# Optimization experiments

Hardware: AMD Instinct MI355X
Metric: run time of the kernel (lower is better)

Reference implementation:

```python
import jax, jax.numpy as jnp
import numpy as np

EPS = 0.001
FLOW_WARP_WEIGHT = 1.0
_GRAY_W = jnp.array([0.299, 0.587, 0.114], dtype=jnp.float32)


def _to_gray(img):
    # img: [B, 3, H, W] -> [B, 1, H, W] luminance
    return jnp.einsum('bchw,c->bhw', img, _GRAY_W.astype(img.dtype))[:, None]


def _resize_bilinear_align_corners(x, h_out, w_out):
    # x: [B, C, H, W] -> [B, C, h_out, w_out], bilinear, align_corners=True
    B, C, H, W = x.shape
    sy = jnp.arange(h_out, dtype=x.dtype) * ((H - 1) / max(h_out - 1, 1))
    sx = jnp.arange(w_out, dtype=x.dtype) * ((W - 1) / max(w_out - 1, 1))
    y0 = jnp.floor(sy).astype(jnp.int32)
    x0 = jnp.floor(sx).astype(jnp.int32)
    y1 = jnp.minimum(y0 + 1, H - 1)
    x1 = jnp.minimum(x0 + 1, W - 1)
    wy = (sy - y0)[:, None]            # [h_out, 1]
    wx = (sx - x0)[None, :]            # [1, w_out]
    # interp along H
    xh = x[:, :, y0, :] * (1.0 - wy)[..., None].squeeze(-1)[None, None] if False else x[:, :, y0, :] * (1.0 - wy) + x[:, :, y1, :] * wy  # [B,C,h_out,W]
    # interp along W
    out = xh[:, :, :, x0] * (1.0 - wx) + xh[:, :, :, x1] * wx
    return out


def _resize_flow_to_image(flow, h_img, w_img):
    flow_uv = flow[:, :2]
    fh, fw = flow_uv.shape[-2:]
    if (fh, fw) == (h_img, w_img):
        return flow_uv
    r = _resize_bilinear_align_corners(flow_uv, h_img, w_img)
    scale = jnp.array([w_img / max(fw, 1), h_img / max(fh, 1)], dtype=flow.dtype)
    return r * scale[None, :, None, None]


def _bilinear_sample_zeros(img, gx, gy):
    # img: [B, 1, H, W]; gx, gy: [B, H, W] pixel coords (align_corners=True)
    B, _, H, W = img.shape
    x0f = jnp.floor(gx)
    y0f = jnp.floor(gy)
    wx = gx - x0f
    wy = gy - y0f
    x0 = x0f.astype(jnp.int32)
    y0 = y0f.astype(jnp.int32)
    b = jnp.arange(B)[:, None, None]

    def gather(yi, xi):
        valid = (xi >= 0) & (xi <= W - 1) & (yi >= 0) & (yi <= H - 1)
        v = img[b, 0, jnp.clip(yi, 0, H - 1), jnp.clip(xi, 0, W - 1)]
        return jnp.where(valid, v, jnp.zeros((), img.dtype))

    v00 = gather(y0, x0)
    v01 = gather(y0, x0 + 1)
    v10 = gather(y0 + 1, x0)
    v11 = gather(y0 + 1, x0 + 1)
    out = (v00 * (1 - wx) * (1 - wy) + v01 * wx * (1 - wy)
           + v10 * (1 - wx) * wy + v11 * wx * wy)
    return out[:, None]  # [B,1,H,W]


def _forward(pred_prev, pred_next, flow_prev_to_next):
    prev_g = _to_gray(pred_prev)   # [B,1,H,W]
    next_g = _to_gray(pred_next)
    B, _, H, W = prev_g.shape
    flow_uv = _resize_flow_to_image(flow_prev_to_next, H, W)  # [B,2,H,W]
    yy, xx = jnp.meshgrid(jnp.arange(H, dtype=prev_g.dtype),
                          jnp.arange(W, dtype=prev_g.dtype), indexing='ij')
    gx = xx[None] + flow_uv[:, 0]  # [B,H,W]
    gy = yy[None] + flow_uv[:, 1]
    valid = ((gx >= 0) & (gx <= W - 1) & (gy >= 0) & (gy <= H - 1)).astype(prev_g.dtype)
    warped = _bilinear_sample_zeros(next_g, gx, gy)  # [B,1,H,W]
    diff = prev_g - warped
    valid_mask = valid[:, None]
    valid_count = jnp.maximum(valid_mask.sum(), 1.0)
    loss_map = jnp.sqrt(diff * diff + EPS * EPS) * valid_mask
    loss = loss_map.sum() / valid_count
    return FLOW_WARP_WEIGHT * loss, loss


def setup_inputs() -> dict:
    key = jax.random.key(0)
    k1, k2, k3 = jax.random.split(key, 3)
    pred_prev = jax.random.uniform(k1, (16, 3, 512, 512), dtype=jnp.float32)
    pred_next = jax.random.uniform(k2, (16, 3, 512, 512), dtype=jnp.float32)
    flow = jax.random.normal(k3, (16, 2, 128, 128), dtype=jnp.float32)
    return {"pred_prev": pred_prev, "pred_next": pred_next, "flow_prev_to_next": flow}


def reference(pred_prev, pred_next, flow_prev_to_next):
    return _forward(pred_prev, pred_next, flow_prev_to_next)
```

## Files before the change

kernel.cpp:

```cpp
#include <hip/hip_runtime.h>


typedef _Float16 half4v __attribute__((ext_vector_type(4)));

constexpr int B  = 16;
constexpr int H  = 512;
constexpr int W  = 512;
constexpr int FH = 128;
constexpr int FW = 128;
constexpr int HW  = H * W;
constexpr int IMG = 3 * HW;
constexpr int FHW = FH * FW;
constexpr float EPS = 0.001f;

constexpr int TX = 64, TY = 32;
constexpr int TW = 120, TH = 80;
constexpr int FROWS  = 10;
constexpr int FLOW_F = 2 * FROWS * FW;

constexpr int NB = 2048;

__device__ __forceinline__ float gray3(const float* __restrict__ img, int off) {
    return 0.299f * img[off] + 0.587f * img[HW + off] + 0.114f * img[2 * HW + off];
}

__global__ __launch_bounds__(256) void loss_kernel(
    const float* __restrict__ prev, const float* __restrict__ nxt,
    const float* __restrict__ flow, double* __restrict__ psum,
    unsigned int* __restrict__ pcnt)
{
    __shared__ __align__(16) _Float16 smh[TW * TH];
    __shared__ __align__(16) float    smf[FLOW_F];

    const int bid = ((blockIdx.x & 7) << 8) | (blockIdx.x >> 3);
    const int b   = bid >> 7;
    const int t   = bid & 127;
    const int tx  = t & 7;
    const int ty  = t >> 3;
    const int x0t = tx * TX;
    const int y0t = ty * TY;

    const float fr = (float)(127.0 / 511.0);
    const int fy_lo = (int)((float)y0t * fr);

    const float* __restrict__ nb = nxt + (long)b * IMG;

    for (int it = threadIdx.x; it < TH * (TW / 4); it += 256) {
        const int r  = it / (TW / 4), c = it - r * (TW / 4);
        const int sy = y0t - 24 + r;
        const int sx = x0t - 24 + c * 4;
        half4v hv = (half4v)0;
        if ((unsigned)sy < (unsigned)H && (unsigned)sx <= (unsigned)(W - 4)) {
            const float* __restrict__ p = nb + sy * W + sx;
            const float4 rr = *(const float4*)(p);
            const float4 gg = *(const float4*)(p + HW);
            const float4 bl = *(const float4*)(p + 2 * HW);
            hv[0] = (_Float16)(0.299f * rr.x + 0.587f * gg.x + 0.114f * bl.x);
            hv[1] = (_Float16)(0.299f * rr.y + 0.587f * gg.y + 0.114f * bl.y);
            hv[2] = (_Float16)(0.299f * rr.z + 0.587f * gg.z + 0.114f * bl.z);
            hv[3] = (_Float16)(0.299f * rr.w + 0.587f * gg.w + 0.114f * bl.w);
        }
        *(half4v*)(smh + r * TW + c * 4) = hv;
    }
    {
        const float* __restrict__ fsrc = flow + (long)b * 2 * FHW;
        for (int it = threadIdx.x; it < 2 * FROWS * (FW / 4); it += 256) {
            const int c    = it / (FROWS * (FW / 4));
            const int rr   = (it - c * (FROWS * (FW / 4))) >> 5;
            const int c4   = it & 31;
            const int frow = min(fy_lo + rr, FH - 1);
            const float4 v = *(const float4*)(fsrc + c * FHW + frow * FW + c4 * 4);
            *(float4*)(smf + c * (FROWS * FW) + rr * FW + c4 * 4) = v;
        }
    }

    const int xq = threadIdx.x & 15;
    const int yl = threadIdx.x >> 4;
    const int xb = x0t + xq * 4;

    float pg[2][4];
    #pragma unroll
    for (int k = 0; k < 2; ++k) {
        const int y = y0t + yl + k * 16;
        const float* __restrict__ pb = prev + (long)b * IMG + y * W + xb;
        const float4 pr  = *(const float4*)(pb);
        const float4 pgc = *(const float4*)(pb + HW);
        const float4 plc = *(const float4*)(pb + 2 * HW);
        pg[k][0] = 0.299f * pr.x + 0.587f * pgc.x + 0.114f * plc.x;
        pg[k][1] = 0.299f * pr.y + 0.587f * pgc.y + 0.114f * plc.y;
        pg[k][2] = 0.299f * pr.z + 0.587f * pgc.z + 0.114f * plc.z;
        pg[k][3] = 0.299f * pr.w + 0.587f * pgc.w + 0.114f * plc.w;
    }

    __syncthreads();

    const float sxfb = (float)xb * fr;
    const int F  = (int)sxfb;
    const int F2 = min(F + 2, FW - 1);

    double lsum = 0.0;
    unsigned int lcnt = 0;

    #pragma unroll
    for (int k = 0; k < 2; ++k) {
        const int y = y0t + yl + k * 16;

        const float syf = (float)y * fr;
        const int   fy0 = (int)syf;
        const float wy  = syf - (float)fy0;
        const int r0 = fy0 - fy_lo;
        const int r1 = min(fy0 + 1, FH - 1) - fy_lo;

        const float* __restrict__ su = smf;
        const float* __restrict__ sv = smf + FROWS * FW;
        const float u0a = su[r0 * FW + F], u0b = su[r0 * FW + F + 1], u0c = su[r0 * FW + F2];
        const float u1a = su[r1 * FW + F], u1b = su[r1 * FW + F + 1], u1c = su[r1 * FW + F2];
        const float v0a = sv[r0 * FW + F], v0b = sv[r0 * FW + F + 1], v0c = sv[r0 * FW + F2];
        const float v1a = sv[r1 * FW + F], v1b = sv[r1 * FW + F + 1], v1c = sv[r1 * FW + F2];

        #pragma unroll
        for (int i = 0; i < 4; ++i) {
            const int x = xb + i;
            const float sxf = (float)x * fr;
            const int   fx0 = (int)sxf;
            const float wx  = sxf - (float)fx0;
            const int   d   = fx0 - F;

            const float u00 = d ? u0b : u0a, u01 = d ? u0c : u0b;
            const float u10 = d ? u1b : u1a, u11 = d ? u1c : u1b;
            const float v00 = d ? v0b : v0a, v01 = d ? v0c : v0b;
            const float v10 = d ? v1b : v1a, v11 = d ? v1c : v1b;

            const float uc0 = u00 * (1.0f - wy) + u10 * wy;
            const float uc1 = u01 * (1.0f - wy) + u11 * wy;
            const float vc0 = v00 * (1.0f - wy) + v10 * wy;
            const float vc1 = v01 * (1.0f - wy) + v11 * wy;
            const float u = (uc0 * (1.0f - wx) + uc1 * wx) * 4.0f;
            const float v = (vc0 * (1.0f - wx) + vc1 * wx) * 4.0f;

            const float gx = (float)x + u;
            const float gy = (float)y + v;
            const float vm = ((gx >= 0.0f) & (gx <= (float)(W - 1)) &
                              (gy >= 0.0f) & (gy <= (float)(H - 1))) ? 1.0f : 0.0f;

            const float gxf = floorf(gx), gyf = floorf(gy);
            const float wwx = gx - gxf,  wwy = gy - gyf;
            const int ix0 = (int)gxf, iy0 = (int)gyf;

            const int cx = ix0 - (x0t - 24);
            const int ry = iy0 - (y0t - 24);
            float c00, c01, c10, c11;
            if ((unsigned)cx <= (unsigned)(TW - 2) && (unsigned)ry <= (unsigned)(TH - 2)) {
                const int la = ry * TW + cx;
                c00 = (float)smh[la];      c01 = (float)smh[la + 1];
                c10 = (float)smh[la + TW]; c11 = (float)smh[la + TW + 1];
            } else {
                const bool vx0g = (ix0 >= 0) & (ix0 < W);
                const bool vx1g = (ix0 + 1 >= 0) & (ix0 + 1 < W);
                const bool vy0g = (iy0 >= 0) & (iy0 < H);
                const bool vy1g = (iy0 + 1 >= 0) & (iy0 + 1 < H);
                const int xc0 = min(max(ix0, 0), W - 1), xc1 = min(max(ix0 + 1, 0), W - 1);
                const int yc0 = min(max(iy0, 0), H - 1), yc1 = min(max(iy0 + 1, 0), H - 1);
                c00 = (vy0g & vx0g) ? gray3(nb, yc0 * W + xc0) : 0.0f;
                c01 = (vy0g & vx1g) ? gray3(nb, yc0 * W + xc1) : 0.0f;
                c10 = (vy1g & vx0g) ? gray3(nb, yc1 * W + xc0) : 0.0f;
                c11 = (vy1g & vx1g) ? gray3(nb, yc1 * W + xc1) : 0.0f;
            }

            const float warped = c00 * (1.0f - wwx) * (1.0f - wwy)
                               + c01 * wwx * (1.0f - wwy)
                               + c10 * (1.0f - wwx) * wwy
                               + c11 * wwx * wwy;
            const float diff = pg[k][i] - warped;
            const float l = sqrtf(diff * diff + EPS * EPS);
            lsum += (double)(l * vm);
            lcnt += (unsigned int)vm;
        }
    }

    #pragma unroll
    for (int off = 32; off > 0; off >>= 1) {
        lsum += __shfl_down(lsum, off);
        lcnt += __shfl_down(lcnt, off);
    }
    __shared__ double s_sum[4];
    __shared__ unsigned int s_cnt[4];
    const int wid = threadIdx.x >> 6, lane = threadIdx.x & 63;
    if (lane == 0) { s_sum[wid] = lsum; s_cnt[wid] = lcnt; }
    __syncthreads();
    if (threadIdx.x == 0) {
        psum[blockIdx.x] = s_sum[0] + s_sum[1] + s_sum[2] + s_sum[3];
        pcnt[blockIdx.x] = s_cnt[0] + s_cnt[1] + s_cnt[2] + s_cnt[3];
    }
}

__global__ __launch_bounds__(256) void reduce_kernel(
    const double* __restrict__ psum, const unsigned int* __restrict__ pcnt,
    int nb, float* __restrict__ out)
{
    double s = 0.0;
    unsigned long long c = 0;
    for (int i = threadIdx.x; i < nb; i += 256) {
        s += psum[i];
        c += (unsigned long long)pcnt[i];
    }
    #pragma unroll
    for (int off = 32; off > 0; off >>= 1) {
        s += __shfl_down(s, off);
        c += __shfl_down(c, off);
    }
    __shared__ double ss[4];
    __shared__ unsigned long long sc[4];
    const int wid = threadIdx.x >> 6, lane = threadIdx.x & 63;
    if (lane == 0) { ss[wid] = s; sc[wid] = c; }
    __syncthreads();
    if (threadIdx.x == 0) {
        double ts = ss[0] + ss[1] + ss[2] + ss[3];
        double tc = (double)(sc[0] + sc[1] + sc[2] + sc[3]);
        if (tc < 1.0) tc = 1.0;
        const float loss = (float)(ts / tc);
        out[0] = loss;
        out[1] = loss;
    }
}

extern "C" void kernel_launch(void* const* d_in, const int* in_sizes, int n_in,
                              void* d_out, int out_size, void* d_ws, size_t ws_size,
                              hipStream_t stream) {
    const float* prev = (const float*)d_in[0];
    const float* nxt  = (const float*)d_in[1];
    const float* flow = (const float*)d_in[2];
    float* out = (float*)d_out;

    double* psum = (double*)d_ws;
    unsigned int* pcnt = (unsigned int*)((char*)d_ws + NB * 8);

    loss_kernel<<<dim3(NB), dim3(256), 0, stream>>>(prev, nxt, flow, psum, pcnt);
    reduce_kernel<<<dim3(1), dim3(256), 0, stream>>>(psum, pcnt, NB, out);
}
```

Baseline: 44.02 us.

## Precompute padded fp16 grayscale of next frame in separate kernel

```diff
diff --git a/kernel.cpp b/kernel.cpp
--- a/kernel.cpp
+++ b/kernel.cpp
@@ -1,7 +1,7 @@
 #include <hip/hip_runtime.h>
 
 
-typedef _Float16 half4v __attribute__((ext_vector_type(4)));
+typedef _Float16 half8 __attribute__((ext_vector_type(8)));
 
 constexpr int B  = 16;
 constexpr int H  = 512;
@@ -13,24 +13,53 @@
 constexpr int FHW = FH * FW;
 constexpr float EPS = 0.001f;
 
+constexpr int P    = 32;
+constexpr int PW   = W + 2 * P;
+constexpr int PH   = H + 2 * P;
+constexpr int PIMG = PW * PH;
+constexpr int PQ8  = PH * (PW / 8);
+
 constexpr int TX = 64, TY = 32;
-constexpr int TW = 120, TH = 80;
-constexpr int FROWS  = 10;
-constexpr int FLOW_F = 2 * FROWS * FW;
+constexpr int TW = 104, TH = 64;
+constexpr int FROWS = 10;
+constexpr int FCOLS = 24;
 
 constexpr int NB = 2048;
 
-__device__ __forceinline__ float gray3(const float* __restrict__ img, int off) {
-    return 0.299f * img[off] + 0.587f * img[HW + off] + 0.114f * img[2 * HW + off];
+__global__ __launch_bounds__(256) void pad_gray_kernel(
+    const float* __restrict__ nxt, _Float16* __restrict__ g)
+{
+    const int q  = blockIdx.x * 256 + threadIdx.x;
+    const int b  = q / PQ8;
+    const int r  = q - b * PQ8;
+    const int py = r / (PW / 8);
+    const int qx = r - py * (PW / 8);
+    const int y  = py - P;
+    const int xs = qx * 8 - P;
+    half8 o = (half8)0;
+    if ((unsigned)y < (unsigned)H && (unsigned)xs <= (unsigned)(W - 8)) {
+        const float* __restrict__ nb = nxt + (long)b * IMG + y * W + xs;
+        #pragma unroll
+        for (int h = 0; h < 2; ++h) {
+            const float4 rr = *(const float4*)(nb + 4 * h);
+            const float4 gg = *(const float4*)(nb + HW + 4 * h);
+            const float4 bl = *(const float4*)(nb + 2 * HW + 4 * h);
+            o[4 * h + 0] = (_Float16)(0.299f * rr.x + 0.587f * gg.x + 0.114f * bl.x);
+            o[4 * h + 1] = (_Float16)(0.299f * rr.y + 0.587f * gg.y + 0.114f * bl.y);
+            o[4 * h + 2] = (_Float16)(0.299f * rr.z + 0.587f * gg.z + 0.114f * bl.z);
+            o[4 * h + 3] = (_Float16)(0.299f * rr.w + 0.587f * gg.w + 0.114f * bl.w);
+        }
+    }
+    *(half8*)(g + (long)b * PIMG + py * PW + qx * 8) = o;
 }
 
 __global__ __launch_bounds__(256) void loss_kernel(
-    const float* __restrict__ prev, const float* __restrict__ nxt,
+    const float* __restrict__ prev, const _Float16* __restrict__ gpad,
     const float* __restrict__ flow, double* __restrict__ psum,
     unsigned int* __restrict__ pcnt)
 {
     __shared__ __align__(16) _Float16 smh[TW * TH];
-    __shared__ __align__(16) float    smf[FLOW_F];
+    __shared__ __align__(16) float    smf[2 * FROWS * FCOLS];
 
     const int bid = ((blockIdx.x & 7) << 8) | (blockIdx.x >> 3);
     const int b   = bid >> 7;
@@ -42,35 +71,25 @@
 
     const float fr = (float)(127.0 / 511.0);
     const int fy_lo = (int)((float)y0t * fr);
-
-    const float* __restrict__ nb = nxt + (long)b * IMG;
-
-    for (int it = threadIdx.x; it < TH * (TW / 4); it += 256) {
-        const int r  = it / (TW / 4), c = it - r * (TW / 4);
-        const int sy = y0t - 24 + r;
-        const int sx = x0t - 24 + c * 4;
-        half4v hv = (half4v)0;
-        if ((unsigned)sy < (unsigned)H && (unsigned)sx <= (unsigned)(W - 4)) {
-            const float* __restrict__ p = nb + sy * W + sx;
-            const float4 rr = *(const float4*)(p);
-            const float4 gg = *(const float4*)(p + HW);
-            const float4 bl = *(const float4*)(p + 2 * HW);
-            hv[0] = (_Float16)(0.299f * rr.x + 0.587f * gg.x + 0.114f * bl.x);
-            hv[1] = (_Float16)(0.299f * rr.y + 0.587f * gg.y + 0.114f * bl.y);
-            hv[2] = (_Float16)(0.299f * rr.z + 0.587f * gg.z + 0.114f * bl.z);
-            hv[3] = (_Float16)(0.299f * rr.w + 0.587f * gg.w + 0.114f * bl.w);
-        }
-        *(half4v*)(smh + r * TW + c * 4) = hv;
-    }
+    const int c0    = min((int)((float)x0t * fr) & ~3, FW - FCOLS);
+
+    const _Float16* __restrict__ gb = gpad + (long)b * PIMG;
+
     {
+        const _Float16* __restrict__ src = gb + (y0t - 16 + P) * PW + (x0t - 16 + P);
+        for (int it = threadIdx.x; it < TH * (TW / 8); it += 256) {
+            const int r = it / (TW / 8), c = it - r * (TW / 8);
+            *(uint4*)(smh + r * TW + c * 8) = *(const uint4*)(src + r * PW + c * 8);
+        }
         const float* __restrict__ fsrc = flow + (long)b * 2 * FHW;
-        for (int it = threadIdx.x; it < 2 * FROWS * (FW / 4); it += 256) {
-            const int c    = it / (FROWS * (FW / 4));
-            const int rr   = (it - c * (FROWS * (FW / 4))) >> 5;
-            const int c4   = it & 31;
+        for (int it = threadIdx.x; it < 2 * FROWS * (FCOLS / 4); it += 256) {
+            const int comp = it / (FROWS * (FCOLS / 4));
+            const int rem  = it - comp * (FROWS * (FCOLS / 4));
+            const int rr   = rem / (FCOLS / 4);
+            const int c4   = rem - rr * (FCOLS / 4);
             const int frow = min(fy_lo + rr, FH - 1);
-            const float4 v = *(const float4*)(fsrc + c * FHW + frow * FW + c4 * 4);
-            *(float4*)(smf + c * (FROWS * FW) + rr * FW + c4 * 4) = v;
+            const float4 v = *(const float4*)(fsrc + comp * FHW + frow * FW + c0 + c4 * 4);
+            *(float4*)(smf + comp * (FROWS * FCOLS) + rr * FCOLS + c4 * 4) = v;
         }
     }
 
@@ -95,8 +114,9 @@
     __syncthreads();
 
     const float sxfb = (float)xb * fr;
-    const int F  = (int)sxfb;
-    const int F2 = min(F + 2, FW - 1);
+    const int F   = (int)sxfb;
+    const int Fl  = F - c0;
+    const int F2l = min(F + 2, FW - 1) - c0;
 
     double lsum = 0.0;
     unsigned int lcnt = 0;
@@ -112,11 +132,11 @@
         const int r1 = min(fy0 + 1, FH - 1) - fy_lo;
 
         const float* __restrict__ su = smf;
-        const float* __restrict__ sv = smf + FROWS * FW;
-        const float u0a = su[r0 * FW + F], u0b = su[r0 * FW + F + 1], u0c = su[r0 * FW + F2];
-        const float u1a = su[r1 * FW + F], u1b = su[r1 * FW + F + 1], u1c = su[r1 * FW + F2];
-        const float v0a = sv[r0 * FW + F], v0b = sv[r0 * FW + F + 1], v0c = sv[r0 * FW + F2];
-        const float v1a = sv[r1 * FW + F], v1b = sv[r1 * FW + F + 1], v1c = sv[r1 * FW + F2];
+        const float* __restrict__ sv = smf + FROWS * FCOLS;
+        const float u0a = su[r0 * FCOLS + Fl], u0b = su[r0 * FCOLS + Fl + 1], u0c = su[r0 * FCOLS + F2l];
+        const float u1a = su[r1 * FCOLS + Fl], u1b = su[r1 * FCOLS + Fl + 1], u1c = su[r1 * FCOLS + F2l];
+        const float v0a = sv[r0 * FCOLS + Fl], v0b = sv[r0 * FCOLS + Fl + 1], v0c = sv[r0 * FCOLS + F2l];
+        const float v1a = sv[r1 * FCOLS + Fl], v1b = sv[r1 * FCOLS + Fl + 1], v1c = sv[r1 * FCOLS + F2l];
 
         #pragma unroll
         for (int i = 0; i < 4; ++i) {
@@ -147,24 +167,19 @@
             const float wwx = gx - gxf,  wwy = gy - gyf;
             const int ix0 = (int)gxf, iy0 = (int)gyf;
 
-            const int cx = ix0 - (x0t - 24);
-            const int ry = iy0 - (y0t - 24);
+            const int cx = ix0 - (x0t - 16);
+            const int ry = iy0 - (y0t - 16);
             float c00, c01, c10, c11;
             if ((unsigned)cx <= (unsigned)(TW - 2) && (unsigned)ry <= (unsigned)(TH - 2)) {
                 const int la = ry * TW + cx;
                 c00 = (float)smh[la];      c01 = (float)smh[la + 1];
                 c10 = (float)smh[la + TW]; c11 = (float)smh[la + TW + 1];
             } else {
-                const bool vx0g = (ix0 >= 0) & (ix0 < W);
-                const bool vx1g = (ix0 + 1 >= 0) & (ix0 + 1 < W);
-                const bool vy0g = (iy0 >= 0) & (iy0 < H);
-                const bool vy1g = (iy0 + 1 >= 0) & (iy0 + 1 < H);
-                const int xc0 = min(max(ix0, 0), W - 1), xc1 = min(max(ix0 + 1, 0), W - 1);
-                const int yc0 = min(max(iy0, 0), H - 1), yc1 = min(max(iy0 + 1, 0), H - 1);
-                c00 = (vy0g & vx0g) ? gray3(nb, yc0 * W + xc0) : 0.0f;
-                c01 = (vy0g & vx1g) ? gray3(nb, yc0 * W + xc1) : 0.0f;
-                c10 = (vy1g & vx0g) ? gray3(nb, yc1 * W + xc0) : 0.0f;
-                c11 = (vy1g & vx1g) ? gray3(nb, yc1 * W + xc1) : 0.0f;
+                const int iyc = min(max(iy0, -P), PH - P - 2);
+                const int ixc = min(max(ix0, -P), PW - P - 2);
+                const _Float16* __restrict__ gp = gb + (iyc + P) * PW + (ixc + P);
+                c00 = (float)gp[0];  c01 = (float)gp[1];
+                c10 = (float)gp[PW]; c11 = (float)gp[PW + 1];
             }
 
             const float warped = c00 * (1.0f - wwx) * (1.0f - wwy)
@@ -196,11 +211,11 @@
 
 __global__ __launch_bounds__(256) void reduce_kernel(
     const double* __restrict__ psum, const unsigned int* __restrict__ pcnt,
-    int nb, float* __restrict__ out)
+    float* __restrict__ out)
 {
     double s = 0.0;
     unsigned long long c = 0;
-    for (int i = threadIdx.x; i < nb; i += 256) {
+    for (int i = threadIdx.x; i < NB; i += 256) {
         s += psum[i];
         c += (unsigned long long)pcnt[i];
     }
@@ -215,7 +230,7 @@
     if (lane == 0) { ss[wid] = s; sc[wid] = c; }
     __syncthreads();
     if (threadIdx.x == 0) {
-        double ts = ss[0] + ss[1] + ss[2] + ss[3];
+        const double ts = ss[0] + ss[1] + ss[2] + ss[3];
         double tc = (double)(sc[0] + sc[1] + sc[2] + sc[3]);
         if (tc < 1.0) tc = 1.0;
         const float loss = (float)(ts / tc);
@@ -234,7 +249,9 @@
 
     double* psum = (double*)d_ws;
     unsigned int* pcnt = (unsigned int*)((char*)d_ws + NB * 8);
-
-    loss_kernel<<<dim3(NB), dim3(256), 0, stream>>>(prev, nxt, flow, psum, pcnt);
-    reduce_kernel<<<dim3(1), dim3(256), 0, stream>>>(psum, pcnt, NB, out);
-}
+    _Float16* gbuf = (_Float16*)((char*)d_ws + 32768);
+
+    pad_gray_kernel<<<dim3(B * PQ8 / 256), dim3(256), 0, stream>>>(nxt, gbuf);
+    loss_kernel<<<dim3(NB), dim3(256), 0, stream>>>(prev, gbuf, flow, psum, pcnt);
+    reduce_kernel<<<dim3(1), dim3(256), 0, stream>>>(psum, pcnt, out);
+}
```

New measurement: 35.75 us. -18.8%, faster.
